# Kernel tuning notes

Hardware: AMD Instinct MI355X
Metric: run time of the kernel (lower is better)

Reference implementation:

```python
import jax, jax.numpy as jnp
import numpy as np

B, T, D, H = 4, 2048, 512, 8
DH = D // H
SCALE = DH ** (-0.5)

def setup_inputs() -> dict:
    key = jax.random.key(0)
    k1, k2, k3 = jax.random.split(key, 3)
    x = jax.random.normal(k1, (B, T, D), dtype=jnp.float32)
    m = jnp.ones((B, T), dtype=jnp.float32)
    w_qkv = jax.random.normal(k2, (D, 3 * D), dtype=jnp.float32) * (D ** -0.5)
    w_out = jax.random.normal(k3, (D, D), dtype=jnp.float32) * (D ** -0.5)
    b_out = jnp.zeros((D,), dtype=jnp.float32)
    return {"x": x, "m": m, "w_qkv": w_qkv, "w_out": w_out, "b_out": b_out}

def reference(x, m, w_qkv, w_out, b_out):
    # qkv projection (no bias), split into heads: b t h d
    qkv = x @ w_qkv                                  # [B,T,3D]
    q, k, v = jnp.split(qkv, 3, axis=-1)
    def heads(t):
        return t.reshape(B, T, H, DH)
    q, k, v = heads(q), heads(k), heads(v)
    # raw scores, layout [b, i, j, h] as in the torch einsum
    e = jnp.einsum('bihd,bjhd->bijh', q, k) * SCALE  # [B,T,T,H]
    # causal + key-padding mask: kpm[b,i,j] = m[b,i]*m[b,j] lower-triangled
    kpm = m[:, :, None] * m[:, None, :]              # [B,T,T]
    kpm = jnp.tril(kpm)
    neg = -jnp.finfo(e.dtype).max
    e = jnp.where(kpm[..., None] == 0, neg, e)
    a = jax.nn.softmax(e, axis=2)                    # softmax over keys j
    o = jnp.einsum('bijh,bjhd->bihd', a, v)          # [B,T,H,DH]
    o = o.reshape(B, T, D)
    o = o @ w_out + b_out
    return o * m[..., None]
```

## Files before the change

### kernel.cpp

```cpp
#include <hip/hip_runtime.h>
#include <hip/hip_bf16.h>
#include <stdint.h>

#define B_ 4
#define T_ 2048
#define D_ 512
#define H_ 8
#define DH_ 64
#define M_TOT (B_*T_)
#define N_QKV (3*D_)
#define QSCALE_ 0.18033688011112043f
#define NEGINF_ -3.0e38f

typedef __attribute__((ext_vector_type(8))) short short8;
typedef __attribute__((ext_vector_type(8))) unsigned short ushort8;
typedef __attribute__((ext_vector_type(4))) unsigned short ushort4_t;
typedef __attribute__((ext_vector_type(4))) float f32x4;
typedef __attribute__((ext_vector_type(16))) float f32x16;

#define MFMA32(a,b,c) __builtin_amdgcn_mfma_f32_32x32x16_bf16(a,b,c,0,0,0)
#define MFMA16(a,b,c) __builtin_amdgcn_mfma_f32_16x16x32_bf16(a,b,c,0,0,0)

static __device__ __forceinline__ unsigned short f2bf(float f) {
    union { float f; unsigned u; } v; v.f = f;
    unsigned r = v.u + 0x7fffu + ((v.u >> 16) & 1u);
    return (unsigned short)(r >> 16);
}

__global__ __launch_bounds__(256) void prep_kernel(
    const float* __restrict__ x, const float* __restrict__ w_qkv,
    const float* __restrict__ w_out, const float* __restrict__ m,
    unsigned short* __restrict__ x_bf, unsigned short* __restrict__ wqkvT,
    unsigned short* __restrict__ woutT, int* __restrict__ padflags)
{
    const int NX  = M_TOT * D_ / 8;
    const int NW1 = D_ * N_QKV;
    const int NW2 = D_ * D_;
    int tid = blockIdx.x * 256 + threadIdx.x;
    if (tid < NX) {
        int i = tid * 8;
        f32x4 a = *(const f32x4*)(x + i);
        f32x4 b = *(const f32x4*)(x + i + 4);
        ushort8 o;
        o[0] = f2bf(a[0]); o[1] = f2bf(a[1]); o[2] = f2bf(a[2]); o[3] = f2bf(a[3]);
        o[4] = f2bf(b[0]); o[5] = f2bf(b[1]); o[6] = f2bf(b[2]); o[7] = f2bf(b[3]);
        *(ushort8*)(x_bf + i) = o;
    } else if (tid < NX + NW1) {
        int idx = tid - NX;
        int k = idx & 511, n = idx >> 9;
        wqkvT[n * 512 + k] = f2bf(w_qkv[k * N_QKV + n]);
    } else if (tid < NX + NW1 + NW2) {
        int idx = tid - NX - NW1;
        int k = idx & 511, n = idx >> 9;
        woutT[n * 512 + k] = f2bf(w_out[k * D_ + n]);
    } else if (tid < NX + NW1 + NW2 + 128) {
        int idx = tid - NX - NW1 - NW2;
        int b = idx >> 5, jt = idx & 31;
        const float* mp = m + b * T_ + jt * 64;
        int any = 0;
#pragma unroll 8
        for (int t = 0; t < 64; ++t) any |= (mp[t] == 0.f) ? 1 : 0;
        padflags[idx] = any;
    }
}

__device__ __forceinline__ void gemm_tile_128(
    const unsigned short* __restrict__ A, const unsigned short* __restrict__ Bt,
    int bm, int bn, unsigned short* sA, unsigned short* sB, f32x4 acc[4][4])
{
    const int tid = threadIdx.x;
    const int w = tid >> 6, l = tid & 63;
    const int wr = (w >> 1) * 64, wc = (w & 1) * 64;
    const int lr = l >> 3, lp = l & 7;
    const int i16 = l & 15, g = l >> 4;
#pragma unroll
    for (int mi = 0; mi < 4; ++mi)
#pragma unroll
        for (int ni = 0; ni < 4; ++ni)
#pragma unroll
            for (int r = 0; r < 4; ++r) acc[mi][ni][r] = 0.f;

    for (int kt = 0; kt < 512; kt += 64) {
#pragma unroll
        for (int i = 0; i < 4; ++i) {
            int r = w * 32 + i * 8 + lr;
            int c = lp ^ (r & 7);
            __builtin_amdgcn_global_load_lds(
                (const __attribute__((address_space(1))) void*)(A + (size_t)(bm + r) * 512 + kt + c * 8),
                (__attribute__((address_space(3))) void*)(sA + (w * 32 + i * 8) * 64),
                16, 0, 0);
            __builtin_amdgcn_global_load_lds(
                (const __attribute__((address_space(1))) void*)(Bt + (size_t)(bn + r) * 512 + kt + c * 8),
                (__attribute__((address_space(3))) void*)(sB + (w * 32 + i * 8) * 64),
                16, 0, 0);
        }
        __syncthreads();
#pragma unroll
        for (int kk = 0; kk < 2; ++kk) {
            short8 af[4], bf2[4];
#pragma unroll
            for (int i = 0; i < 4; ++i) {
                int ra = wr + i * 16 + i16;
                af[i]  = *(const short8*)(sA + ra * 64 + (((kk * 4 + g) ^ (ra & 7)) * 8));
                int rb = wc + i * 16 + i16;
                bf2[i] = *(const short8*)(sB + rb * 64 + (((kk * 4 + g) ^ (rb & 7)) * 8));
            }
#pragma unroll
            for (int mi = 0; mi < 4; ++mi)
#pragma unroll
                for (int ni = 0; ni < 4; ++ni)
                    acc[mi][ni] = MFMA16(af[mi], bf2[ni], acc[mi][ni]);
        }
        __syncthreads();
    }
}

__global__ __launch_bounds__(256) void gemm_qkv_kernel(
    const unsigned short* __restrict__ A, const unsigned short* __restrict__ Bt,
    unsigned short* __restrict__ qkv, unsigned short* __restrict__ vT)
{
    __shared__ __align__(16) unsigned short sA[128 * 64];
    __shared__ __align__(16) unsigned short sB[128 * 64];
    f32x4 acc[4][4];
    int bn = blockIdx.x * 128, bm = blockIdx.y * 128;
    gemm_tile_128(A, Bt, bm, bn, sA, sB, acc);
    const int l = threadIdx.x & 63, w = threadIdx.x >> 6;
    const int wr = (w >> 1) * 64, wc = (w & 1) * 64;
    if (bn < 1024) {
        bool isQ = (bn < 512);
#pragma unroll
        for (int mi = 0; mi < 4; ++mi)
#pragma unroll
            for (int ni = 0; ni < 4; ++ni)
#pragma unroll
                for (int r = 0; r < 4; ++r) {
                    int row = bm + wr + mi * 16 + (l >> 4) * 4 + r;
                    int col = bn + wc + ni * 16 + (l & 15);
                    float v = acc[mi][ni][r];
                    if (isQ) v *= QSCALE_;
                    qkv[(size_t)row * N_QKV + col] = f2bf(v);
                }
    } else {
#pragma unroll
        for (int mi = 0; mi < 4; ++mi)
#pragma unroll
            for (int ni = 0; ni < 4; ++ni) {
                int row0 = bm + wr + mi * 16 + (l >> 4) * 4;
                int dall = bn - 1024 + wc + ni * 16 + (l & 15);
                int hh = dall >> 6, d = dall & 63;
                int b = row0 >> 11, t0 = row0 & 2047;
                ushort4_t vv;
#pragma unroll
                for (int r = 0; r < 4; ++r) vv[r] = f2bf(acc[mi][ni][r]);
                *(ushort4_t*)(vT + ((size_t)((b * 8 + hh) * 64 + d)) * T_ + t0) = vv;
            }
    }
}

__global__ __launch_bounds__(256) void gemm_out_kernel(
    const unsigned short* __restrict__ A, const unsigned short* __restrict__ Bt,
    const float* __restrict__ b_out, const float* __restrict__ m,
    float* __restrict__ out)
{
    __shared__ __align__(16) unsigned short sA[128 * 64];
    __shared__ __align__(16) unsigned short sB[128 * 64];
    f32x4 acc[4][4];
    int bn = blockIdx.x * 128, bm = blockIdx.y * 128;
    gemm_tile_128(A, Bt, bm, bn, sA, sB, acc);
    const int l = threadIdx.x & 63, w = threadIdx.x >> 6;
    const int wr = (w >> 1) * 64, wc = (w & 1) * 64;
#pragma unroll
    for (int mi = 0; mi < 4; ++mi)
#pragma unroll
        for (int ni = 0; ni < 4; ++ni)
#pragma unroll
            for (int r = 0; r < 4; ++r) {
                int row = bm + wr + mi * 16 + (l >> 4) * 4 + r;
                int col = bn + wc + ni * 16 + (l & 15);
                out[(size_t)row * D_ + col] = (acc[mi][ni][r] + b_out[col]) * m[row];
            }
}

__global__ __launch_bounds__(256) void attn_kernel(
    const unsigned short* __restrict__ qkv, const unsigned short* __restrict__ vT,
    const float* __restrict__ m, const int* __restrict__ padflags,
    unsigned short* __restrict__ o_bf)
{
    __shared__ __align__(16) char smem[33280];
    unsigned short* sK0 = (unsigned short*)smem;
    unsigned short* sK1 = (unsigned short*)(smem + 8192);
    unsigned short* sV0 = (unsigned short*)(smem + 16384);
    unsigned short* sV1 = (unsigned short*)(smem + 24576);
    float* sBias = (float*)(smem + 32768);
    float* sMrgO = (float*)smem;
    float* sMrgS = (float*)(smem + 16896);

    const int tid = threadIdx.x, wv = tid >> 6, l = tid & 63;
    const int i31 = l & 31, hl = l >> 5;
    const int kvpar = wv >> 1;
    const int rb = wv & 1;
    const int bh = blockIdx.x, bb = bh >> 3, h = bh & 7;
    const int q = 31 - (int)blockIdx.y;
    const int qb = q * 64;
    const int qrow = qb + rb * 32 + i31;
    const int swz = i31 & 7;
    const int lr = l >> 3, lp = l & 7, cst = lp ^ lr;
    const int kv_s = wv & 1, kvp_s = wv >> 1;

    short8 bq[4];
#pragma unroll
    for (int c = 0; c < 4; ++c)
        bq[c] = *(const short8*)(qkv + (size_t)(bb * T_ + qrow) * N_QKV
                                 + h * 64 + c * 16 + hl * 8);

    f32x16 oacc0, oacc1;
#pragma unroll
    for (int rr = 0; rr < 16; ++rr) { oacc0[rr] = 0.f; oacc1[rr] = 0.f; }
    float mrun = -1e30f, lrun = 0.f;

    const int nss = (q >> 1) + 1;
#pragma unroll 1
    for (int ss = 0; ss < nss; ++ss) {
        const int jtA = 2 * ss, jtB = 2 * ss + 1;
        const bool hasB = (jtB <= q);
        const int pfA = padflags[bb * 32 + jtA];
        const int pfB = hasB ? padflags[bb * 32 + jtB] : 0;
        {
            int jtn = 2 * ss + kvp_s;
            if (jtn <= q) {
                char* dst0 = smem + kv_s * 16384 + kvp_s * 8192;
                if (kv_s == 0) {
                    const unsigned short* src = qkv + (size_t)(bb * T_ + jtn * 64 + lr) * N_QKV
                                                + 512 + h * 64 + cst * 8;
#pragma unroll
                    for (int is = 0; is < 8; ++is)
                        __builtin_amdgcn_global_load_lds(
                            (const __attribute__((address_space(1))) void*)(src + (size_t)is * 8 * N_QKV),
                            (__attribute__((address_space(3))) void*)(dst0 + is * 1024), 16, 0, 0);
                } else {
                    const unsigned short* src = vT + (size_t)(bh * 64 + lr) * T_
                                                + jtn * 64 + cst * 8;
#pragma unroll
                    for (int is = 0; is < 8; ++is)
                        __builtin_amdgcn_global_load_lds(
                            (const __attribute__((address_space(1))) void*)(src + (size_t)is * 8 * T_),
                            (__attribute__((address_space(3))) void*)(dst0 + is * 1024), 16, 0, 0);
                }
            }
            if (tid < 128) {
                int tI = tid >> 6, jl = tid & 63;
                int pf = tI ? pfB : pfA;
                if (pf) {
                    int jt = tI ? jtB : jtA;
                    sBias[tI * 64 + jl] = (m[bb * T_ + jt * 64 + jl] != 0.f) ? 0.f : NEGINF_;
                }
            }
        }
        asm volatile("s_waitcnt vmcnt(0)" ::: "memory");
        __syncthreads();

        const int jt = kvpar ? jtB : jtA;
        const int pf = kvpar ? pfB : pfA;
        if (kvpar == 0 || hasB) {
            const int j0 = jt * 64;
            const unsigned short* sKp = kvpar ? sK1 : sK0;
            const unsigned short* sVp = kvpar ? sV1 : sV0;

            f32x16 s0, s1;
#pragma unroll
            for (int rr = 0; rr < 16; ++rr) { s0[rr] = 0.f; s1[rr] = 0.f; }
            __builtin_amdgcn_s_setprio(1);
#pragma unroll
            for (int c = 0; c < 4; ++c) {
                int pc = ((2 * c + hl) ^ swz) * 8;
                short8 ka0 = *(const short8*)(sKp + i31 * 64 + pc);
                short8 ka1 = *(const short8*)(sKp + (32 + i31) * 64 + pc);
                s0 = MFMA32(ka0, bq[c], s0);
                s1 = MFMA32(ka1, bq[c], s1);
            }
            __builtin_amdgcn_s_setprio(0);

            if (jt == q) {
#pragma unroll
                for (int qd = 0; qd < 4; ++qd)
#pragma unroll
                    for (int e = 0; e < 4; ++e) {
                        int jl0 = 8 * qd + 4 * hl + e;
                        if (j0 + jl0 > qrow)      s0[qd * 4 + e] = NEGINF_;
                        if (j0 + 32 + jl0 > qrow) s1[qd * 4 + e] = NEGINF_;
                    }
            }
            if (pf) {
#pragma unroll
                for (int qd = 0; qd < 4; ++qd) {
                    f32x4 b0 = *(const f32x4*)(&sBias[kvpar * 64 + 8 * qd + 4 * hl]);
                    f32x4 b1 = *(const f32x4*)(&sBias[kvpar * 64 + 32 + 8 * qd + 4 * hl]);
#pragma unroll
                    for (int e = 0; e < 4; ++e) {
                        s0[qd * 4 + e] += b0[e];
                        s1[qd * 4 + e] += b1[e];
                    }
                }
            }

            float pm = NEGINF_;
#pragma unroll
            for (int rr = 0; rr < 16; ++rr)
                pm = fmaxf(pm, fmaxf(s0[rr], s1[rr]));
            pm = fmaxf(pm, __shfl_xor(pm, 32, 64));
            if (__all(pm - mrun <= 8.f)) {
                float ls = 0.f;
#pragma unroll
                for (int rr = 0; rr < 16; ++rr) {
                    float p0 = __builtin_amdgcn_exp2f(s0[rr] - mrun);
                    float p1 = __builtin_amdgcn_exp2f(s1[rr] - mrun);
                    s0[rr] = p0; s1[rr] = p1;
                    ls += p0 + p1;
                }
                ls += __shfl_xor(ls, 32, 64);
                lrun += ls;
            } else {
                float mnew = fmaxf(mrun, pm);
                float scl = __builtin_amdgcn_exp2f(mrun - mnew);
                mrun = mnew;
                float ls = 0.f;
#pragma unroll
                for (int rr = 0; rr < 16; ++rr) {
                    float p0 = __builtin_amdgcn_exp2f(s0[rr] - mnew);
                    float p1 = __builtin_amdgcn_exp2f(s1[rr] - mnew);
                    s0[rr] = p0; s1[rr] = p1;
                    ls += p0 + p1;
                }
                ls += __shfl_xor(ls, 32, 64);
                lrun = lrun * scl + ls;
#pragma unroll
                for (int rr = 0; rr < 16; ++rr) { oacc0[rr] *= scl; oacc1[rr] *= scl; }
            }

            unsigned int pw0[8], pw1[8];
#pragma unroll
            for (int k2 = 0; k2 < 8; ++k2) {
                unsigned int wa, wb;
                asm("v_cvt_pk_bf16_f32 %0, %1, %2" : "=v"(wa) : "v"(s0[2 * k2]), "v"(s0[2 * k2 + 1]));
                asm("v_cvt_pk_bf16_f32 %0, %1, %2" : "=v"(wb) : "v"(s1[2 * k2]), "v"(s1[2 * k2 + 1]));
                pw0[k2] = wa; pw1[k2] = wb;
            }
            asm("v_permlane32_swap_b32 %0, %1" : "+v"(pw0[0]), "+v"(pw0[2]));
            asm("v_permlane32_swap_b32 %0, %1" : "+v"(pw0[1]), "+v"(pw0[3]));
            asm("v_permlane32_swap_b32 %0, %1" : "+v"(pw0[4]), "+v"(pw0[6]));
            asm("v_permlane32_swap_b32 %0, %1" : "+v"(pw0[5]), "+v"(pw0[7]));
            asm("v_permlane32_swap_b32 %0, %1" : "+v"(pw1[0]), "+v"(pw1[2]));
            asm("v_permlane32_swap_b32 %0, %1" : "+v"(pw1[1]), "+v"(pw1[3]));
            asm("v_permlane32_swap_b32 %0, %1" : "+v"(pw1[4]), "+v"(pw1[6]));
            asm("v_permlane32_swap_b32 %0, %1" : "+v"(pw1[5]), "+v"(pw1[7]));
            union PU { unsigned int u[4]; short8 s8; };
            PU pb[4];
            pb[0].u[0] = pw0[0]; pb[0].u[1] = pw0[1]; pb[0].u[2] = pw0[2]; pb[0].u[3] = pw0[3];
            pb[1].u[0] = pw0[4]; pb[1].u[1] = pw0[5]; pb[1].u[2] = pw0[6]; pb[1].u[3] = pw0[7];
            pb[2].u[0] = pw1[0]; pb[2].u[1] = pw1[1]; pb[2].u[2] = pw1[2]; pb[2].u[3] = pw1[3];
            pb[3].u[0] = pw1[4]; pb[3].u[1] = pw1[5]; pb[3].u[2] = pw1[6]; pb[3].u[3] = pw1[7];

            __builtin_amdgcn_s_setprio(1);
#pragma unroll
            for (int c = 0; c < 4; ++c) {
                int pc = ((2 * c + hl) ^ swz) * 8;
                short8 va0 = *(const short8*)(sVp + i31 * 64 + pc);
                short8 va1 = *(const short8*)(sVp + (32 + i31) * 64 + pc);
                oacc0 = MFMA32(va0, pb[c].s8, oacc0);
                oacc1 = MFMA32(va1, pb[c].s8, oacc1);
            }
            __builtin_amdgcn_s_setprio(0);
        }
        __syncthreads();
    }

    if (kvpar == 1) {
#pragma unroll
        for (int rr = 0; rr < 16; ++rr) {
            sMrgO[(rb * 64 + l) * 33 + rr]      = oacc0[rr];
            sMrgO[(rb * 64 + l) * 33 + 16 + rr] = oacc1[rr];
        }
        sMrgS[(rb * 64 + l) * 2 + 0] = mrun;
        sMrgS[(rb * 64 + l) * 2 + 1] = lrun;
    }
    __syncthreads();
    if (kvpar == 0) {
        float mB = sMrgS[(rb * 64 + l) * 2 + 0], lB = sMrgS[(rb * 64 + l) * 2 + 1];
        float ms = fmaxf(mrun, mB);
        float sA2 = __builtin_amdgcn_exp2f(mrun - ms);
        float sB2 = __builtin_amdgcn_exp2f(mB - ms);
        float lt = lrun * sA2 + lB * sB2;
        float rinv = (lt > 0.f) ? 1.0f / lt : 0.f;
#pragma unroll
        for (int td = 0; td < 2; ++td)
#pragma unroll
            for (int qd = 0; qd < 4; ++qd) {
                ushort4_t o4;
#pragma unroll
                for (int e = 0; e < 4; ++e) {
                    float mine = td ? oacc1[qd * 4 + e] : oacc0[qd * 4 + e];
                    float ov = (mine * sA2 + sMrgO[(rb * 64 + l) * 33 + td * 16 + qd * 4 + e] * sB2) * rinv;
                    o4[e] = f2bf(ov);
                }
                *(ushort4_t*)(o_bf + (size_t)(bb * T_ + qrow) * D_
                              + h * 64 + 32 * td + 8 * qd + 4 * hl) = o4;
            }
    }
}

extern "C" void kernel_launch(void* const* d_in, const int* in_sizes, int n_in,
                              void* d_out, int out_size, void* d_ws, size_t ws_size,
                              hipStream_t stream)
{
    const float* x     = (const float*)d_in[0];
    const float* m     = (const float*)d_in[1];
    const float* w_qkv = (const float*)d_in[2];
    const float* w_out = (const float*)d_in[3];
    const float* b_out = (const float*)d_in[4];
    float* out = (float*)d_out;

    char* ws = (char*)d_ws;
    unsigned short* x_bf   = (unsigned short*)(ws);
    unsigned short* wqkvT  = (unsigned short*)(ws + 8388608);
    unsigned short* woutT  = (unsigned short*)(ws + 9961472);
    unsigned short* qkv_bf = (unsigned short*)(ws + 10485760);
    unsigned short* o_bf   = (unsigned short*)(ws + 35651584);
    unsigned short* vT     = (unsigned short*)d_out;
    int* padflags          = (int*)((char*)d_out + 8388608);

    hipLaunchKernelGGL(prep_kernel, dim3(6145), dim3(256), 0, stream,
                       x, w_qkv, w_out, m, x_bf, wqkvT, woutT, padflags);
    hipLaunchKernelGGL(gemm_qkv_kernel, dim3(12, 64), dim3(256), 0, stream,
                       x_bf, wqkvT, qkv_bf, vT);
    hipLaunchKernelGGL(attn_kernel, dim3(32, 32), dim3(256), 0, stream,
                       qkv_bf, vT, m, padflags, o_bf);
    hipLaunchKernelGGL(gemm_out_kernel, dim3(4, 64), dim3(256), 0, stream,
                       o_bf, woutT, b_out, m, out);
}
```

Before: 95.79 us.

## Double-buffer K/V tiles in attention and precompute padding bias globally

The attention loop now uses two 32KB LDS buffers. The K/V tiles for the next step are issued with global_load_lds while the current step computes, hiding load latency instead of waiting on vmcnt before every iteration. The per-iteration shared-memory mask bias is replaced by a global bias array filled once in the prep kernel. Shared memory per block doubles to 64KB, which lowers attention occupancy. Correctness depends on barriers and waitcnts that are not visible in the shown lines.

New measurement: 101.0 us. +5.4%, slower.

```diff
diff --git a/kernel.cpp b/kernel.cpp
--- a/kernel.cpp
+++ b/kernel.cpp
@@ -31,7 +31,8 @@
     const float* __restrict__ x, const float* __restrict__ w_qkv,
     const float* __restrict__ w_out, const float* __restrict__ m,
     unsigned short* __restrict__ x_bf, unsigned short* __restrict__ wqkvT,
-    unsigned short* __restrict__ woutT, int* __restrict__ padflags)
+    unsigned short* __restrict__ woutT, int* __restrict__ padflags,
+    float* __restrict__ bias_g)
 {
     const int NX  = M_TOT * D_ / 8;
     const int NW1 = D_ * N_QKV;
@@ -61,6 +62,9 @@
 #pragma unroll 8
         for (int t = 0; t < 64; ++t) any |= (mp[t] == 0.f) ? 1 : 0;
         padflags[idx] = any;
+    } else if (tid < NX + NW1 + NW2 + 128 + M_TOT) {
+        int idx = tid - NX - NW1 - NW2 - 128;
+        bias_g[idx] = (m[idx] != 0.f) ? 0.f : NEGINF_;
     }
 }
 
@@ -183,15 +187,10 @@
 
 __global__ __launch_bounds__(256) void attn_kernel(
     const unsigned short* __restrict__ qkv, const unsigned short* __restrict__ vT,
-    const float* __restrict__ m, const int* __restrict__ padflags,
+    const float* __restrict__ bias_g, const int* __restrict__ padflags,
     unsigned short* __restrict__ o_bf)
 {
-    __shared__ __align__(16) char smem[33280];
-    unsigned short* sK0 = (unsigned short*)smem;
-    unsigned short* sK1 = (unsigned short*)(smem + 8192);
-    unsigned short* sV0 = (unsigned short*)(smem + 16384);
-    unsigned short* sV1 = (unsigned short*)(smem + 24576);
-    float* sBias = (float*)(smem + 32768);
+    __shared__ __align__(16) char smem[65536];
     float* sMrgO = (float*)smem;
     float* sMrgS = (float*)(smem + 16896);
 
@@ -218,53 +217,46 @@
     for (int rr = 0; rr < 16; ++rr) { oacc0[rr] = 0.f; oacc1[rr] = 0.f; }
     float mrun = -1e30f, lrun = 0.f;
 
+    auto STAGE = [&](int ssn, int buf) {
+        int jtn = 2 * ssn + kvp_s;
+        if (jtn <= q) {
+            char* dst0 = smem + buf * 32768 + kvp_s * 16384 + kv_s * 8192;
+            if (kv_s == 0) {
+                const unsigned short* src = qkv + (size_t)(bb * T_ + jtn * 64 + lr) * N_QKV
+                                            + 512 + h * 64 + cst * 8;
+#pragma unroll
+                for (int is = 0; is < 8; ++is)
+                    __builtin_amdgcn_global_load_lds(
+                        (const __attribute__((address_space(1))) void*)(src + (size_t)is * 8 * N_QKV),
+                        (__attribute__((address_space(3))) void*)(dst0 + is * 1024), 16, 0, 0);
+            } else {
+                const unsigned short* src = vT + (size_t)(bh * 64 + lr) * T_
+                                            + jtn * 64 + cst * 8;
+#pragma unroll
+                for (int is = 0; is < 8; ++is)
+                    __builtin_amdgcn_global_load_lds(
+                        (const __attribute__((address_space(1))) void*)(src + (size_t)is * 8 * T_),
+                        (__attribute__((address_space(3))) void*)(dst0 + is * 1024), 16, 0, 0);
+            }
+        }
+    };
+
     const int nss = (q >> 1) + 1;
+    STAGE(0, 0);
+    __syncthreads();
+
 #pragma unroll 1
     for (int ss = 0; ss < nss; ++ss) {
-        const int jtA = 2 * ss, jtB = 2 * ss + 1;
-        const bool hasB = (jtB <= q);
-        const int pfA = padflags[bb * 32 + jtA];
-        const int pfB = hasB ? padflags[bb * 32 + jtB] : 0;
-        {
-            int jtn = 2 * ss + kvp_s;
-            if (jtn <= q) {
-                char* dst0 = smem + kv_s * 16384 + kvp_s * 8192;
-                if (kv_s == 0) {
-                    const unsigned short* src = qkv + (size_t)(bb * T_ + jtn * 64 + lr) * N_QKV
-                                                + 512 + h * 64 + cst * 8;
-#pragma unroll
-                    for (int is = 0; is < 8; ++is)
-                        __builtin_amdgcn_global_load_lds(
-                            (const __attribute__((address_space(1))) void*)(src + (size_t)is * 8 * N_QKV),
-                            (__attribute__((address_space(3))) void*)(dst0 + is * 1024), 16, 0, 0);
-                } else {
-                    const unsigned short* src = vT + (size_t)(bh * 64 + lr) * T_
-                                                + jtn * 64 + cst * 8;
-#pragma unroll
-                    for (int is = 0; is < 8; ++is)
-                        __builtin_amdgcn_global_load_lds(
-                            (const __attribute__((address_space(1))) void*)(src + (size_t)is * 8 * T_),
-                            (__attribute__((address_space(3))) void*)(dst0 + is * 1024), 16, 0, 0);
-                }
-            }
-            if (tid < 128) {
-                int tI = tid >> 6, jl = tid & 63;
-                int pf = tI ? pfB : pfA;
-                if (pf) {
-                    int jt = tI ? jtB : jtA;
-                    sBias[tI * 64 + jl] = (m[bb * T_ + jt * 64 + jl] != 0.f) ? 0.f : NEGINF_;
-                }
-            }
-        }
-        asm volatile("s_waitcnt vmcnt(0)" ::: "memory");
-        __syncthreads();
-
-        const int jt = kvpar ? jtB : jtA;
-        const int pf = kvpar ? pfB : pfA;
+        const int cur = ss & 1;
+        if (ss + 1 < nss) STAGE(ss + 1, cur ^ 1);
+
+        const int jt = 2 * ss + kvpar;
+        const bool hasB = (2 * ss + 1 <= q);
         if (kvpar == 0 || hasB) {
             const int j0 = jt * 64;
-            const unsigned short* sKp = kvpar ? sK1 : sK0;
-            const unsigned short* sVp = kvpar ? sV1 : sV0;
+            const unsigned short* sKp = (const unsigned short*)(smem + cur * 32768 + kvpar * 16384);
+            const unsigned short* sVp = (const unsigned short*)(smem + cur * 32768 + kvpar * 16384 + 8192);
+            const int pf = padflags[bb * 32 + jt];
 
             f32x16 s0, s1;
 #pragma unroll
@@ -293,8 +285,8 @@
             if (pf) {
 #pragma unroll
                 for (int qd = 0; qd < 4; ++qd) {
-                    f32x4 b0 = *(const f32x4*)(&sBias[kvpar * 64 + 8 * qd + 4 * hl]);
-                    f32x4 b1 = *(const f32x4*)(&sBias[kvpar * 64 + 32 + 8 * qd + 4 * hl]);
+                    f32x4 b0 = *(const f32x4*)(bias_g + bb * T_ + j0 + 8 * qd + 4 * hl);
+                    f32x4 b1 = *(const f32x4*)(bias_g + bb * T_ + j0 + 32 + 8 * qd + 4 * hl);
 #pragma unroll
                     for (int e = 0; e < 4; ++e) {
                         s0[qd * 4 + e] += b0[e];
@@ -427,13 +419,14 @@
     unsigned short* o_bf   = (unsigned short*)(ws + 35651584);
     unsigned short* vT     = (unsigned short*)d_out;
     int* padflags          = (int*)((char*)d_out + 8388608);
-
-    hipLaunchKernelGGL(prep_kernel, dim3(6145), dim3(256), 0, stream,
-                       x, w_qkv, w_out, m, x_bf, wqkvT, woutT, padflags);
+    float* bias_g          = (float*)((char*)d_out + 8390656);
+
+    hipLaunchKernelGGL(prep_kernel, dim3(6177), dim3(256), 0, stream,
+                       x, w_qkv, w_out, m, x_bf, wqkvT, woutT, padflags, bias_g);
     hipLaunchKernelGGL(gemm_qkv_kernel, dim3(12, 64), dim3(256), 0, stream,
                        x_bf, wqkvT, qkv_bf, vT);
     hipLaunchKernelGGL(attn_kernel, dim3(32, 32), dim3(256), 0, stream,
-                       qkv_bf, vT, m, padflags, o_bf);
+                       qkv_bf, vT, bias_g, padflags, o_bf);
     hipLaunchKernelGGL(gemm_out_kernel, dim3(4, 64), dim3(256), 0, stream,
                        o_bf, woutT, b_out, m, out);
 }
```

## Tile weight transposes through LDS and remap GEMM blocks across XCDs

Applied to the files above, without the earlier changes.

The prep kernel's weight transpose-and-convert now reads 64x64 tiles with vectorized coalesced loads, transposes them through padded shared memory, and writes 16-byte bf16 chunks. Before, each thread handled one element with strided scalar accesses. This shrinks the prep grid from 6145 to 2305 blocks. Both GEMM kernels also remap block IDs so consecutive tiles land on the same XCD, aiming for better L2 reuse of shared A/B tiles, at the cost of a small index computation.

Measured after the change: 94.62 us. No clear change (-1.2%).

```diff
diff --git a/kernel.cpp b/kernel.cpp
--- a/kernel.cpp
+++ b/kernel.cpp
@@ -33,34 +33,51 @@
     unsigned short* __restrict__ x_bf, unsigned short* __restrict__ wqkvT,
     unsigned short* __restrict__ woutT, int* __restrict__ padflags)
 {
-    const int NX  = M_TOT * D_ / 8;
-    const int NW1 = D_ * N_QKV;
-    const int NW2 = D_ * D_;
-    int tid = blockIdx.x * 256 + threadIdx.x;
-    if (tid < NX) {
-        int i = tid * 8;
+    __shared__ unsigned short sT[64 * 65];
+    const int blk = blockIdx.x, tid = threadIdx.x;
+    if (blk < 2048) {
+        int i = (blk * 256 + tid) * 8;
         f32x4 a = *(const f32x4*)(x + i);
         f32x4 b = *(const f32x4*)(x + i + 4);
         ushort8 o;
         o[0] = f2bf(a[0]); o[1] = f2bf(a[1]); o[2] = f2bf(a[2]); o[3] = f2bf(a[3]);
         o[4] = f2bf(b[0]); o[5] = f2bf(b[1]); o[6] = f2bf(b[2]); o[7] = f2bf(b[3]);
         *(ushort8*)(x_bf + i) = o;
-    } else if (tid < NX + NW1) {
-        int idx = tid - NX;
-        int k = idx & 511, n = idx >> 9;
-        wqkvT[n * 512 + k] = f2bf(w_qkv[k * N_QKV + n]);
-    } else if (tid < NX + NW1 + NW2) {
-        int idx = tid - NX - NW1;
-        int k = idx & 511, n = idx >> 9;
-        woutT[n * 512 + k] = f2bf(w_out[k * D_ + n]);
-    } else if (tid < NX + NW1 + NW2 + 128) {
-        int idx = tid - NX - NW1 - NW2;
-        int b = idx >> 5, jt = idx & 31;
-        const float* mp = m + b * T_ + jt * 64;
-        int any = 0;
+    } else if (blk < 2304) {
+        const bool isQ = (blk < 2240);
+        const int bt = isQ ? (blk - 2048) : (blk - 2240);
+        const int W  = isQ ? N_QKV : D_;
+        const int TX = isQ ? 24 : 8;
+        const float* src = isQ ? w_qkv : w_out;
+        unsigned short* dst = isQ ? wqkvT : woutT;
+        const int n0 = (bt % TX) * 64, k0 = (bt / TX) * 64;
+#pragma unroll
+        for (int p = 0; p < 4; ++p) {
+            int r = p * 16 + (tid >> 4);
+            int c4 = (tid & 15) * 4;
+            f32x4 v = *(const f32x4*)(src + (size_t)(k0 + r) * W + n0 + c4);
+#pragma unroll
+            for (int e = 0; e < 4; ++e) sT[r * 65 + c4 + e] = f2bf(v[e]);
+        }
+        __syncthreads();
+#pragma unroll
+        for (int p = 0; p < 2; ++p) {
+            int nn = p * 32 + (tid >> 3);
+            int kk = (tid & 7) * 8;
+            ushort8 o;
+#pragma unroll
+            for (int e = 0; e < 8; ++e) o[e] = sT[(kk + e) * 65 + nn];
+            *(ushort8*)(dst + (size_t)(n0 + nn) * 512 + k0 + kk) = o;
+        }
+    } else {
+        if (tid < 128) {
+            int b = tid >> 5, jt = tid & 31;
+            const float* mp = m + b * T_ + jt * 64;
+            int any = 0;
 #pragma unroll 8
-        for (int t = 0; t < 64; ++t) any |= (mp[t] == 0.f) ? 1 : 0;
-        padflags[idx] = any;
+            for (int t = 0; t < 64; ++t) any |= (mp[t] == 0.f) ? 1 : 0;
+            padflags[tid] = any;
+        }
     }
 }
 
@@ -115,6 +132,13 @@
     }
 }
 
+static __device__ __forceinline__ void xcd_tile(int gx, int* bx, int* by) {
+    int orig = blockIdx.y * gx + blockIdx.x;
+    int nwg = gx * gridDim.y;
+    int wgid = (orig & 7) * (nwg >> 3) + (orig >> 3);
+    *bx = wgid % gx; *by = wgid / gx;
+}
+
 __global__ __launch_bounds__(256) void gemm_qkv_kernel(
     const unsigned short* __restrict__ A, const unsigned short* __restrict__ Bt,
     unsigned short* __restrict__ qkv, unsigned short* __restrict__ vT)
@@ -122,7 +146,8 @@
     __shared__ __align__(16) unsigned short sA[128 * 64];
     __shared__ __align__(16) unsigned short sB[128 * 64];
     f32x4 acc[4][4];
-    int bn = blockIdx.x * 128, bm = blockIdx.y * 128;
+    int bx, by; xcd_tile(12, &bx, &by);
+    int bn = bx * 128, bm = by * 128;
     gemm_tile_128(A, Bt, bm, bn, sA, sB, acc);
     const int l = threadIdx.x & 63, w = threadIdx.x >> 6;
     const int wr = (w >> 1) * 64, wc = (w & 1) * 64;
@@ -165,7 +190,8 @@
     __shared__ __align__(16) unsigned short sA[128 * 64];
     __shared__ __align__(16) unsigned short sB[128 * 64];
     f32x4 acc[4][4];
-    int bn = blockIdx.x * 128, bm = blockIdx.y * 128;
+    int bx, by; xcd_tile(4, &bx, &by);
+    int bn = bx * 128, bm = by * 128;
     gemm_tile_128(A, Bt, bm, bn, sA, sB, acc);
     const int l = threadIdx.x & 63, w = threadIdx.x >> 6;
     const int wr = (w >> 1) * 64, wc = (w & 1) * 64;
@@ -428,7 +454,7 @@
     unsigned short* vT     = (unsigned short*)d_out;
     int* padflags          = (int*)((char*)d_out + 8388608);
 
-    hipLaunchKernelGGL(prep_kernel, dim3(6145), dim3(256), 0, stream,
+    hipLaunchKernelGGL(prep_kernel, dim3(2305), dim3(256), 0, stream,
                        x, w_qkv, w_out, m, x_bf, wqkvT, woutT, padflags);
     hipLaunchKernelGGL(gemm_qkv_kernel, dim3(12, 64), dim3(256), 0, stream,
                        x_bf, wqkvT, qkv_bf, vT);
```
